# Optimization experiments

Hardware: AMD Instinct MI355X
Metric: run time of the kernel (lower is better)

The kernel has to match this reference:

```python
import jax, jax.numpy as jnp
import numpy as np

NUM_LAYERS = 24
LN_EPS = 1e-5


def setup_inputs() -> dict:
    key = jax.random.key(0)
    ks = jax.random.split(key, 8)
    B, S = 256, 8192
    x = jax.random.uniform(ks[0], (B, S, 5), dtype=jnp.float32)
    # per-layer LayerNorm(4) params (torch default init: weight=1, bias=0; use
    # randomized values so the gather is non-trivial)
    ln_w = 1.0 + 0.1 * jax.random.normal(ks[1], (NUM_LAYERS, 4), dtype=jnp.float32)
    ln_b = 0.1 * jax.random.normal(ks[2], (NUM_LAYERS, 4), dtype=jnp.float32)
    # MLP 5 -> 64 -> 32 -> 1 (dropout inactive in eval mode)
    W1 = jax.random.normal(ks[3], (64, 5), dtype=jnp.float32) / np.sqrt(5)
    b1 = jnp.zeros((64,), dtype=jnp.float32)
    W2 = jax.random.normal(ks[4], (32, 64), dtype=jnp.float32) / np.sqrt(64)
    b2 = jnp.zeros((32,), dtype=jnp.float32)
    W3 = jax.random.normal(ks[5], (1, 32), dtype=jnp.float32) / np.sqrt(32)
    b3 = jnp.zeros((1,), dtype=jnp.float32)
    return {"x": x, "ln_w": ln_w, "ln_b": ln_b, "W1": W1, "b1": b1,
            "W2": W2, "b2": b2, "W3": W3, "b3": b3}


def reference(x, ln_w, ln_b, W1, b1, W2, b2, W3, b3):
    B, S, _ = x.shape
    x_flat = x.reshape(-1, 5)                      # [N, 5]
    layer_pos = x_flat[:, -1]                      # [N]
    layer_ids = jnp.clip((layer_pos * NUM_LAYERS).astype(jnp.int32), 0, NUM_LAYERS - 1)
    feats = x_flat[:, :4]                          # [N, 4]
    # vectorized per-token LayerNorm: gather per-token gamma/beta by layer id
    mean = jnp.mean(feats, axis=-1, keepdims=True)
    var = jnp.mean(jnp.square(feats - mean), axis=-1, keepdims=True)  # biased, as torch LN
    normed = (feats - mean) * jax.lax.rsqrt(var + LN_EPS)
    normed = normed * ln_w[layer_ids] + ln_b[layer_ids]               # [N, 4]
    x_norm = jnp.concatenate([normed, layer_pos[:, None]], axis=1)    # [N, 5]
    h = jax.nn.relu(x_norm @ W1.T + b1)            # [N, 64]
    h = jax.nn.relu(h @ W2.T + b2)                 # [N, 32]
    scores = h @ W3.T + b3                         # [N, 1]
    return scores.reshape(B, S)
```

## Files before the change

### kernel.cpp

```cpp
#include <hip/hip_runtime.h>
#include <hip/hip_bf16.h>
#include <stdint.h>

#define NUM_LAYERS 24
#define LN_EPS 1e-5f
#define N_ROWS (256 * 8192)
#define ROWS_PER_ITER 64
#define NUM_ITERS (N_ROWS / ROWS_PER_ITER)
#define NUM_BLOCKS 2048

typedef __attribute__((ext_vector_type(8)))  short bf16x8;
typedef __attribute__((ext_vector_type(16))) float f32x16;
typedef __attribute__((ext_vector_type(2)))  float f32x2;

__device__ __forceinline__ uint32_t pk_bf16(float lo, float hi) {
    __hip_bfloat162 h2 = __float22bfloat162_rn(float2{lo, hi});
    uint32_t u;
    __builtin_memcpy(&u, &h2, 4);
    return u;
}

union FragU { bf16x8 f; uint32_t u[4]; };

__device__ __forceinline__ bf16x8 make_frag(uint32_t d0, uint32_t d1,
                                            uint32_t d2, uint32_t d3) {
    FragU fu;
    fu.u[0] = d0; fu.u[1] = d1; fu.u[2] = d2; fu.u[3] = d3;
    return fu.f;
}

__device__ __forceinline__ int sigma_k(int p) {
    int hh = (p >> 2) & 1;
    int base = (p & 31) - 4 * hh;
    int r = (base & 3) + 4 * (base >> 3);
    return 32 * (p >> 5) + 16 * (r >> 3) + 8 * hh + (r & 7);
}

__global__ __launch_bounds__(256, 3) void router_mfma(
    const float* __restrict__ x,
    const float* __restrict__ ln_w,
    const float* __restrict__ ln_b,
    const float* __restrict__ W1,
    const float* __restrict__ b1,
    const float* __restrict__ W2,
    const float* __restrict__ b2,
    const float* __restrict__ W3,
    const float* __restrict__ b3,
    float* __restrict__ out)
{
    __shared__ float s_ln[NUM_LAYERS * 8];
    const int t = threadIdx.x;
    if (t < NUM_LAYERS * 4) {
        int lid = t >> 2, c = t & 3;
        s_ln[lid * 8 + c]     = ln_w[t];
        s_ln[lid * 8 + 4 + c] = ln_b[t];
    }
    __syncthreads();

    const int lane = t & 63;
    const int wid  = t >> 6;
    const int n32  = lane & 31;
    const int h    = lane >> 5;

    bf16x8 a1f[2];
#pragma unroll
    for (int mt = 0; mt < 2; ++mt) {
        int p = mt * 32 + n32;
        int k = sigma_k(p);
        float w0 = W1[k * 5 + 0], w1 = W1[k * 5 + 1], w2 = W1[k * 5 + 2];
        float w3 = W1[k * 5 + 3], w4 = W1[k * 5 + 4];
        float bc = b1[k];
        uint32_t d0 = pk_bf16(w0, w1);
        uint32_t d1 = pk_bf16(w2, w3);
        uint32_t d2 = pk_bf16(w4, bc);
        if (h) { d0 = 0; d1 = 0; d2 = 0; }
        a1f[mt] = make_frag(d0, d1, d2, 0);
    }

    bf16x8 w2f[4];
#pragma unroll
    for (int kt = 0; kt < 4; ++kt) {
        const float* wp = W2 + n32 * 64 + kt * 16 + h * 8;
        const float4 lo = *(const float4*)(wp);
        const float4 hi = *(const float4*)(wp + 4);
        w2f[kt] = make_frag(pk_bf16(lo.x, lo.y), pk_bf16(lo.z, lo.w),
                            pk_bf16(hi.x, hi.y), pk_bf16(hi.z, hi.w));
    }

    f32x2 w3p[8], b2p[8];
#pragma unroll
    for (int r2 = 0; r2 < 8; ++r2) {
        const int r = 2 * r2;
        const int n = (r & 3) + 8 * (r >> 2) + 4 * h;
        w3p[r2] = f32x2{W3[n], W3[n + 1]};
        b2p[r2] = f32x2{b2[n], b2[n + 1]};
    }
    const float b3v = b3[0];

    f32x16 zf;
#pragma unroll
    for (int i = 0; i < 16; ++i) zf[i] = 0.0f;
    const f32x2 z2 = {0.0f, 0.0f};

    const int total_waves = NUM_BLOCKS * 4;
    const int w = blockIdx.x * 4 + wid;

    int it = w;
    const float* xp0 = x + (size_t)(it * ROWS_PER_ITER + lane) * 5;
    float f0 = xp0[0], f1 = xp0[1], f2 = xp0[2], f3 = xp0[3], lp = xp0[4];

    while (true) {
        const int nit = it + total_waves;
        const bool more = nit < NUM_ITERS;
        const float* nxp =
            x + (size_t)((more ? nit : it) * ROWS_PER_ITER + lane) * 5;
        const float nf0 = nxp[0], nf1 = nxp[1], nf2 = nxp[2], nf3 = nxp[3],
                    nlp = nxp[4];

        const int rowBase = it * ROWS_PER_ITER;

        int lid = (int)(lp * (float)NUM_LAYERS);
        lid = lid < 0 ? 0 : (lid > NUM_LAYERS - 1 ? NUM_LAYERS - 1 : lid);

        const float m  = (f0 + f1 + f2 + f3) * 0.25f;
        const float d0 = f0 - m, d1 = f1 - m, d2 = f2 - m, d3 = f3 - m;
        const float var = (d0 * d0 + d1 * d1 + d2 * d2 + d3 * d3) * 0.25f;
        const float r   = rsqrtf(var + LN_EPS);

        const float4 g  = *(const float4*)(s_ln + lid * 8);
        const float4 bb = *(const float4*)(s_ln + lid * 8 + 4);

        const float xn0 = fmaf(d0 * r, g.x, bb.x);
        const float xn1 = fmaf(d1 * r, g.y, bb.y);
        const float xn2 = fmaf(d2 * r, g.z, bb.z);
        const float xn3 = fmaf(d3 * r, g.w, bb.w);

        const uint32_t e0 = pk_bf16(xn0, xn1);
        const uint32_t e1 = pk_bf16(xn2, xn3);
        const uint32_t e2 = pk_bf16(lp, 1.0f);
        const uint32_t x0 = __shfl_xor((int)e0, 32, 64);
        const uint32_t x1 = __shfl_xor((int)e1, 32, 64);
        const uint32_t x2 = __shfl_xor((int)e2, 32, 64);

        const bf16x8 bf_t0 = make_frag(h ? 0u : e0, h ? 0u : e1, h ? 0u : e2, 0u);
        const bf16x8 bf_t1 = make_frag(h ? 0u : x0, h ? 0u : x1, h ? 0u : x2, 0u);

        float res[2];
#pragma unroll
        for (int tile = 0; tile < 2; ++tile) {
            const bf16x8 b1f = tile ? bf_t1 : bf_t0;

            f32x16 c1a = __builtin_amdgcn_mfma_f32_32x32x16_bf16(a1f[0], b1f, zf, 0, 0, 0);
            f32x16 c1b = __builtin_amdgcn_mfma_f32_32x32x16_bf16(a1f[1], b1f, zf, 0, 0, 0);

            bf16x8 h1f[4];
#pragma unroll
            for (int kt = 0; kt < 4; ++kt) {
                const f32x16& c1 = (kt < 2) ? c1a : c1b;
                const int roff = 8 * (kt & 1);
                uint32_t dw[4];
#pragma unroll
                for (int d = 0; d < 4; ++d) {
                    f32x2 v = {c1[roff + 2 * d], c1[roff + 2 * d + 1]};
                    v = __builtin_elementwise_max(v, z2);
                    dw[d] = pk_bf16(v.x, v.y);
                }
                h1f[kt] = make_frag(dw[0], dw[1], dw[2], dw[3]);
            }

            f32x16 c2 = __builtin_amdgcn_mfma_f32_32x32x16_bf16(w2f[0], h1f[0], zf, 0, 0, 0);
#pragma unroll
            for (int kt = 1; kt < 4; ++kt)
                c2 = __builtin_amdgcn_mfma_f32_32x32x16_bf16(w2f[kt], h1f[kt], c2, 0, 0, 0);

            f32x2 acc = z2;
#pragma unroll
            for (int r2 = 0; r2 < 8; ++r2) {
                f32x2 v = {c2[2 * r2], c2[2 * r2 + 1]};
                v = v + b2p[r2];
                v = __builtin_elementwise_max(v, z2);
                acc = v * w3p[r2] + acc;
            }
            float part = acc.x + acc.y;
            part += __shfl_xor(part, 32, 64);
            res[tile] = part + b3v;
        }

        out[rowBase + lane] = (h ? res[1] : res[0]) + 0.0f;

        if (!more) break;
        it = nit;
        f0 = nf0; f1 = nf1; f2 = nf2; f3 = nf3; lp = nlp;
    }
}

extern "C" void kernel_launch(void* const* d_in, const int* in_sizes, int n_in,
                              void* d_out, int out_size, void* d_ws, size_t ws_size,
                              hipStream_t stream) {
    const float* x    = (const float*)d_in[0];
    const float* ln_w = (const float*)d_in[1];
    const float* ln_b = (const float*)d_in[2];
    const float* W1   = (const float*)d_in[3];
    const float* b1   = (const float*)d_in[4];
    const float* W2   = (const float*)d_in[5];
    const float* b2   = (const float*)d_in[6];
    const float* W3   = (const float*)d_in[7];
    const float* b3   = (const float*)d_in[8];
    float* out = (float*)d_out;

    router_mfma<<<NUM_BLOCKS, 256, 0, stream>>>(x, ln_w, ln_b, W1, b1, W2, b2,
                                                W3, b3, out);
}
```

Measured before the change: 117.7 us.

## Switch MFMA path from bf16 to fp16 with packed RTZ conversion and inline asm

Replaces bf16 MFMA with fp16 MFMA issued through inline asm, and uses the hardware v_cvt_pkrtz instruction to pack activations instead of the multi-instruction bf16 RNE conversion. ReLU on the hidden layer is now applied as a packed fp16 max after conversion. The b2 bias is folded into the MFMA accumulator init, b3 is added once after the tile select, and the h-lane zero masking on B fragments is dropped because the A fragments are already zero there. The cost is manual s_nop hazard fences around the asm MFMAs, which may over-serialize, plus fp16 range and RTZ rounding risks on intermediate values.

```diff
diff --git a/kernel.cpp b/kernel.cpp
--- a/kernel.cpp
+++ b/kernel.cpp
@@ -9,24 +9,51 @@
 #define NUM_ITERS (N_ROWS / ROWS_PER_ITER)
 #define NUM_BLOCKS 2048
 
-typedef __attribute__((ext_vector_type(8)))  short bf16x8;
-typedef __attribute__((ext_vector_type(16))) float f32x16;
-typedef __attribute__((ext_vector_type(2)))  float f32x2;
-
-__device__ __forceinline__ uint32_t pk_bf16(float lo, float hi) {
-    __hip_bfloat162 h2 = __float22bfloat162_rn(float2{lo, hi});
-    uint32_t u;
-    __builtin_memcpy(&u, &h2, 4);
+typedef __attribute__((ext_vector_type(4)))  uint32_t u32x4;
+typedef __attribute__((ext_vector_type(16))) float    f32x16;
+typedef __attribute__((ext_vector_type(2)))  float    f32x2;
+typedef __attribute__((ext_vector_type(2)))  __fp16   h16x2;
+
+__device__ __forceinline__ uint32_t pk_f16_rtz(float lo, float hi) {
+    h16x2 v = __builtin_amdgcn_cvt_pkrtz(lo, hi);
+    uint32_t u; __builtin_memcpy(&u, &v, 4);
     return u;
 }
-
-union FragU { bf16x8 f; uint32_t u[4]; };
-
-__device__ __forceinline__ bf16x8 make_frag(uint32_t d0, uint32_t d1,
-                                            uint32_t d2, uint32_t d3) {
-    FragU fu;
-    fu.u[0] = d0; fu.u[1] = d1; fu.u[2] = d2; fu.u[3] = d3;
-    return fu.f;
+__device__ __forceinline__ uint32_t pk_f16_rne(float lo, float hi) {
+    __fp16 a = (__fp16)lo, b = (__fp16)hi;
+    uint16_t ua, ub;
+    __builtin_memcpy(&ua, &a, 2); __builtin_memcpy(&ub, &b, 2);
+    return (uint32_t)ua | ((uint32_t)ub << 16);
+}
+__device__ __forceinline__ uint32_t pk_relu_f16(uint32_t d) {
+    h16x2 v; __builtin_memcpy(&v, &d, 4);
+    h16x2 z = {(__fp16)0.0f, (__fp16)0.0f};
+    v = __builtin_elementwise_max(v, z);
+    uint32_t u; __builtin_memcpy(&u, &v, 4);
+    return u;
+}
+
+__device__ __forceinline__ u32x4 make_frag(uint32_t d0, uint32_t d1,
+                                           uint32_t d2, uint32_t d3) {
+    u32x4 f; f.x = d0; f.y = d1; f.z = d2; f.w = d3;
+    return f;
+}
+
+__device__ __forceinline__ f32x16 mfma_f16_c(u32x4 a, u32x4 b, const f32x16& c) {
+    f32x16 d;
+    asm("s_nop 2\n\tv_mfma_f32_32x32x16_f16 %0, %1, %2, %3"
+        : "=&v"(d) : "v"(a), "v"(b), "v"(c));
+    return d;
+}
+__device__ __forceinline__ void mfma_f16_acc(f32x16& c, u32x4 a, u32x4 b) {
+    asm("s_nop 2\n\tv_mfma_f32_32x32x16_f16 %0, %1, %2, %0"
+        : "+v"(c) : "v"(a), "v"(b));
+}
+__device__ __forceinline__ void mfma_fence(f32x16& c) {
+    asm volatile("s_nop 7\n\ts_nop 7\n\ts_nop 7" : "+v"(c));
+}
+__device__ __forceinline__ void mfma_fence2(f32x16& c0, f32x16& c1) {
+    asm volatile("s_nop 7\n\ts_nop 7\n\ts_nop 7" : "+v"(c0), "+v"(c1));
 }
 
 __device__ __forceinline__ int sigma_k(int p) {
@@ -62,38 +89,36 @@
     const int n32  = lane & 31;
     const int h    = lane >> 5;
 
-    bf16x8 a1f[2];
+    u32x4 a1f[2];
 #pragma unroll
     for (int mt = 0; mt < 2; ++mt) {
         int p = mt * 32 + n32;
         int k = sigma_k(p);
-        float w0 = W1[k * 5 + 0], w1 = W1[k * 5 + 1], w2 = W1[k * 5 + 2];
-        float w3 = W1[k * 5 + 3], w4 = W1[k * 5 + 4];
-        float bc = b1[k];
-        uint32_t d0 = pk_bf16(w0, w1);
-        uint32_t d1 = pk_bf16(w2, w3);
-        uint32_t d2 = pk_bf16(w4, bc);
+        uint32_t d0 = pk_f16_rne(W1[k * 5 + 0], W1[k * 5 + 1]);
+        uint32_t d1 = pk_f16_rne(W1[k * 5 + 2], W1[k * 5 + 3]);
+        uint32_t d2 = pk_f16_rne(W1[k * 5 + 4], b1[k]);
         if (h) { d0 = 0; d1 = 0; d2 = 0; }
         a1f[mt] = make_frag(d0, d1, d2, 0);
     }
 
-    bf16x8 w2f[4];
+    u32x4 w2f[4];
 #pragma unroll
     for (int kt = 0; kt < 4; ++kt) {
         const float* wp = W2 + n32 * 64 + kt * 16 + h * 8;
         const float4 lo = *(const float4*)(wp);
         const float4 hi = *(const float4*)(wp + 4);
-        w2f[kt] = make_frag(pk_bf16(lo.x, lo.y), pk_bf16(lo.z, lo.w),
-                            pk_bf16(hi.x, hi.y), pk_bf16(hi.z, hi.w));
-    }
-
-    f32x2 w3p[8], b2p[8];
+        w2f[kt] = make_frag(pk_f16_rne(lo.x, lo.y), pk_f16_rne(lo.z, lo.w),
+                            pk_f16_rne(hi.x, hi.y), pk_f16_rne(hi.z, hi.w));
+    }
+
+    f32x16 c2init;
+    f32x2 w3p[8];
 #pragma unroll
     for (int r2 = 0; r2 < 8; ++r2) {
-        const int r = 2 * r2;
-        const int n = (r & 3) + 8 * (r >> 2) + 4 * h;
+        const int n = ((2 * r2) & 3) + 8 * (r2 >> 1) + 4 * h;
         w3p[r2] = f32x2{W3[n], W3[n + 1]};
-        b2p[r2] = f32x2{b2[n], b2[n + 1]};
+        c2init[2 * r2]     = b2[n];
+        c2init[2 * r2 + 1] = b2[n + 1];
     }
     const float b3v = b3[0];
 
@@ -135,58 +160,57 @@
         const float xn2 = fmaf(d2 * r, g.z, bb.z);
         const float xn3 = fmaf(d3 * r, g.w, bb.w);
 
-        const uint32_t e0 = pk_bf16(xn0, xn1);
-        const uint32_t e1 = pk_bf16(xn2, xn3);
-        const uint32_t e2 = pk_bf16(lp, 1.0f);
+        const uint32_t e0 = pk_f16_rtz(xn0, xn1);
+        const uint32_t e1 = pk_f16_rtz(xn2, xn3);
+        const uint32_t e2 = pk_f16_rtz(lp, 1.0f);
         const uint32_t x0 = __shfl_xor((int)e0, 32, 64);
         const uint32_t x1 = __shfl_xor((int)e1, 32, 64);
         const uint32_t x2 = __shfl_xor((int)e2, 32, 64);
 
-        const bf16x8 bf_t0 = make_frag(h ? 0u : e0, h ? 0u : e1, h ? 0u : e2, 0u);
-        const bf16x8 bf_t1 = make_frag(h ? 0u : x0, h ? 0u : x1, h ? 0u : x2, 0u);
+        const u32x4 bf_t0 = make_frag(e0, e1, e2, 0u);
+        const u32x4 bf_t1 = make_frag(x0, x1, x2, 0u);
 
         float res[2];
 #pragma unroll
         for (int tile = 0; tile < 2; ++tile) {
-            const bf16x8 b1f = tile ? bf_t1 : bf_t0;
-
-            f32x16 c1a = __builtin_amdgcn_mfma_f32_32x32x16_bf16(a1f[0], b1f, zf, 0, 0, 0);
-            f32x16 c1b = __builtin_amdgcn_mfma_f32_32x32x16_bf16(a1f[1], b1f, zf, 0, 0, 0);
-
-            bf16x8 h1f[4];
+            const u32x4 b1f = tile ? bf_t1 : bf_t0;
+
+            f32x16 c1a = mfma_f16_c(a1f[0], b1f, zf);
+            f32x16 c1b = mfma_f16_c(a1f[1], b1f, zf);
+            mfma_fence2(c1a, c1b);
+
+            u32x4 h1f[4];
 #pragma unroll
             for (int kt = 0; kt < 4; ++kt) {
                 const f32x16& c1 = (kt < 2) ? c1a : c1b;
                 const int roff = 8 * (kt & 1);
                 uint32_t dw[4];
 #pragma unroll
-                for (int d = 0; d < 4; ++d) {
-                    f32x2 v = {c1[roff + 2 * d], c1[roff + 2 * d + 1]};
-                    v = __builtin_elementwise_max(v, z2);
-                    dw[d] = pk_bf16(v.x, v.y);
-                }
+                for (int d = 0; d < 4; ++d)
+                    dw[d] = pk_relu_f16(
+                        pk_f16_rtz(c1[roff + 2 * d], c1[roff + 2 * d + 1]));
                 h1f[kt] = make_frag(dw[0], dw[1], dw[2], dw[3]);
             }
 
-            f32x16 c2 = __builtin_amdgcn_mfma_f32_32x32x16_bf16(w2f[0], h1f[0], zf, 0, 0, 0);
+            f32x16 c2 = mfma_f16_c(w2f[0], h1f[0], c2init);
 #pragma unroll
             for (int kt = 1; kt < 4; ++kt)
-                c2 = __builtin_amdgcn_mfma_f32_32x32x16_bf16(w2f[kt], h1f[kt], c2, 0, 0, 0);
+                mfma_f16_acc(c2, w2f[kt], h1f[kt]);
+            mfma_fence(c2);
 
             f32x2 acc = z2;
 #pragma unroll
             for (int r2 = 0; r2 < 8; ++r2) {
                 f32x2 v = {c2[2 * r2], c2[2 * r2 + 1]};
-                v = v + b2p[r2];
                 v = __builtin_elementwise_max(v, z2);
                 acc = v * w3p[r2] + acc;
             }
             float part = acc.x + acc.y;
             part += __shfl_xor(part, 32, 64);
-            res[tile] = part + b3v;
+            res[tile] = part;
         }
 
-        out[rowBase + lane] = (h ? res[1] : res[0]) + 0.0f;
+        out[rowBase + lane] = (h ? res[1] : res[0]) + b3v;
 
         if (!more) break;
         it = nit;
```

Result: faster. 109.5 us (-6.9%).
